# Kernel optimization log

Measured on AMD Instinct MI355X. Metric: run time of the kernel, lower is better.

The kernel has to match this reference:

```python
import jax, jax.numpy as jnp
import numpy as np

N_NODES = 50000
N_EDGES = 1600000
IN_DIM = 128
OUT_DIM = 128


def setup_inputs() -> dict:
    key = jax.random.key(0)
    k_h, k_e, k_wm, k_wu, k_bu = jax.random.split(key, 5)
    h = jax.random.normal(k_h, (N_NODES, IN_DIM), dtype=jnp.float32)
    edge_index = jax.random.randint(k_e, (2, N_EDGES), 0, N_NODES, dtype=jnp.int64)
    # nn.Linear weights: W_msg [out, in] no bias; W_upd [out, in+out] with bias
    s1 = 1.0 / np.sqrt(IN_DIM)
    s2 = 1.0 / np.sqrt(IN_DIM + OUT_DIM)
    W_msg = jax.random.uniform(k_wm, (OUT_DIM, IN_DIM), jnp.float32, -s1, s1)
    W_upd = jax.random.uniform(k_wu, (OUT_DIM, IN_DIM + OUT_DIM), jnp.float32, -s2, s2)
    b_upd = jax.random.uniform(k_bu, (OUT_DIM,), jnp.float32, -s2, s2)
    return {"h": h, "edge_index": edge_index, "W_msg": W_msg, "W_upd": W_upd, "b_upd": b_upd}


def reference(h, edge_index, W_msg, W_upd, b_upd):
    src, dst = edge_index[0], edge_index[1]
    # gather -> linear: messages [E, out_dim]
    messages = jnp.einsum("ei,oi->eo", h[src], W_msg)
    # scatter-add aggregation into [N, out_dim]
    agg = jax.ops.segment_sum(messages, dst, num_segments=h.shape[0])
    # concat -> linear -> relu
    hu = jnp.concatenate([h, agg], axis=1)
    return jax.nn.relu(jnp.einsum("ni,oi->no", hu, W_upd) + b_upd)
```

## Files before the change

### kernel.cpp

```cpp
#include <hip/hip_runtime.h>
#include <hip/hip_bf16.h>

#define NN   50000
#define NE   1600000
#define D    128
#define NBUK 391
#define CAP  5120
#define EPB  4096
#define ASTR 136
#define PREP_BLKS 3125
#define WPREP_BLKS 32

typedef __attribute__((ext_vector_type(8))) short short8;
typedef __attribute__((ext_vector_type(4))) float f32x4;

__device__ __forceinline__ unsigned short f2b(float x) {
  unsigned u = __float_as_uint(x);
  u += 0x7fffu + ((u >> 16) & 1u);
  return (unsigned short)(u >> 16);
}
__device__ __forceinline__ float b2f(unsigned v) {
  return __uint_as_float(v << 16);
}
__device__ __forceinline__ float b2fh(unsigned v) {
  return __uint_as_float(v & 0xffff0000u);
}

__global__ __launch_bounds__(512) void fused_k(const float* __restrict__ h,
                                               unsigned short* __restrict__ hb,
                                               int* __restrict__ gcur,
                                               const float* __restrict__ Wm,
                                               const float* __restrict__ Wu,
                                               unsigned short* __restrict__ W1b,
                                               unsigned short* __restrict__ Wcb,
                                               const int* __restrict__ ei,
                                               unsigned* __restrict__ ebuf) {
  __shared__ int cnt[NBUK];
  __shared__ int off[NBUK];
  __shared__ int nz;
  const int blk = blockIdx.x, tid = threadIdx.x;

  if (blk >= NBUK) {
    if (blk < NBUK + PREP_BLKS) {
      int i = (blk - NBUK) * 512 + tid;
      float4 x = ((const float4*)h)[i];
      ushort4 o;
      o.x = f2b(x.x); o.y = f2b(x.y); o.z = f2b(x.z); o.w = f2b(x.w);
      ((ushort4*)hb)[i] = o;
    } else {
      int t2 = (blk - NBUK - PREP_BLKS) * 512 + tid;
      if (t2 < 16384) {
        int o = t2 >> 7, j = t2 & 127;
        W1b[t2] = f2b(Wu[o * 256 + j]);
        float acc = 0.f;
#pragma unroll 4
        for (int k = 0; k < 128; ++k)
          acc += Wu[o * 256 + 128 + k] * Wm[k * 128 + j];
        Wcb[t2] = f2b(acc);
      }
    }
    return;
  }

  if (tid == 0) nz = 0;
  if (tid < NBUK) cnt[tid] = 0;
  __syncthreads();
  if (tid < 256) {
    int idx = 1 + 2 * (tid * (NE / 256));
    if (ei[idx] != 0) atomicOr(&nz, 1);
  }
  __syncthreads();
  const int f = (nz == 0);

  const int e0 = blk * EPB + tid * 8;
  unsigned pk[8]; int bk[8]; int lr[8];
  if (e0 + 8 <= NE) {
    int sv[8], dv[8];
    if (f) {
      const int4* ps = (const int4*)(ei + 2 * (size_t)e0);
      const int4* pd = (const int4*)(ei + 2 * (size_t)NE + 2 * (size_t)e0);
      int4 a = ps[0], b = ps[1], c = ps[2], d = ps[3];
      sv[0]=a.x; sv[1]=a.z; sv[2]=b.x; sv[3]=b.z; sv[4]=c.x; sv[5]=c.z; sv[6]=d.x; sv[7]=d.z;
      a = pd[0]; b = pd[1]; c = pd[2]; d = pd[3];
      dv[0]=a.x; dv[1]=a.z; dv[2]=b.x; dv[3]=b.z; dv[4]=c.x; dv[5]=c.z; dv[6]=d.x; dv[7]=d.z;
    } else {
      const int4* ps = (const int4*)(ei + e0);
      const int4* pd = (const int4*)(ei + (size_t)NE + e0);
      int4 a = ps[0], b = ps[1];
      sv[0]=a.x; sv[1]=a.y; sv[2]=a.z; sv[3]=a.w; sv[4]=b.x; sv[5]=b.y; sv[6]=b.z; sv[7]=b.w;
      a = pd[0]; b = pd[1];
      dv[0]=a.x; dv[1]=a.y; dv[2]=a.z; dv[3]=a.w; dv[4]=b.x; dv[5]=b.y; dv[6]=b.z; dv[7]=b.w;
    }
#pragma unroll
    for (int j = 0; j < 8; ++j) {
      bk[j] = dv[j] >> 7;
      pk[j] = (unsigned)sv[j] | ((unsigned)(dv[j] & 127) << 16);
      lr[j] = atomicAdd(&cnt[bk[j]], 1);
    }
  } else {
    for (int j = 0; j < 8; ++j) {
      int e = e0 + j;
      bk[j] = -1;
      if (e < NE) {
        int src = f ? ei[2 * (size_t)e] : ei[e];
        int dst = f ? ei[2 * ((size_t)NE + e)] : ei[NE + e];
        bk[j] = dst >> 7;
        pk[j] = (unsigned)src | ((unsigned)(dst & 127) << 16);
        lr[j] = atomicAdd(&cnt[bk[j]], 1);
      }
    }
  }
  __syncthreads();
  if (tid < NBUK)
    off[tid] = cnt[tid] ? atomicAdd(&gcur[tid], cnt[tid]) : 0;
  __syncthreads();
#pragma unroll
  for (int j = 0; j < 8; ++j) {
    if (bk[j] >= 0) {
      int idx = off[bk[j]] + lr[j];
      if (idx < CAP) ebuf[(size_t)bk[j] * CAP + idx] = pk[j];
    }
  }
}

__global__ __launch_bounds__(512, 6) void sortagg_k(const unsigned* __restrict__ ebuf,
                                                    const int* __restrict__ gcur,
                                                    const unsigned short* __restrict__ hb,
                                                    const unsigned short* __restrict__ W1b,
                                                    const unsigned short* __restrict__ Wcb,
                                                    const float* __restrict__ bias,
                                                    float* __restrict__ out) {
  __shared__ unsigned short srt[CAP];
  __shared__ __align__(16) unsigned short aggL[128 * ASTR];
  __shared__ int cnt[128];
  __shared__ int ofs[129];
  __shared__ int cur[128];
  __shared__ int wsum[2];
  const int b = blockIdx.x, tid = threadIdx.x;
  const int lane = tid & 63, wv = tid >> 6;
  if (tid < 128) cnt[tid] = 0;
  __syncthreads();
  const int count = min(gcur[b], CAP);
  const unsigned* eb = ebuf + (size_t)b * CAP;
  for (int e = tid; e < count; e += 512)
    atomicAdd(&cnt[eb[e] >> 16], 1);
  __syncthreads();
  int v = 0, s = 0;
  if (tid < 128) {
    v = cnt[tid]; s = v;
#pragma unroll
    for (int d = 1; d < 64; d <<= 1) {
      int t = __shfl_up(s, d, 64);
      if (lane >= d) s += t;
    }
    if (lane == 63) wsum[wv] = s;
  }
  __syncthreads();
  if (tid < 128) {
    int excl = (wv ? wsum[0] : 0) + s - v;
    ofs[tid] = excl;
    cur[tid] = excl;
  }
  if (tid == 0) ofs[128] = count;
  __syncthreads();
  for (int e = tid; e < count; e += 512) {
    unsigned p = eb[e];
    int slot = atomicAdd(&cur[p >> 16], 1);
    srt[slot] = (unsigned short)(p & 0xffffu);
  }
  __syncthreads();

  const int q = lane >> 4;
  const int r = lane & 15;
  const unsigned short* hbl = hb + r * 8;
#pragma unroll 1
  for (int k = 0; k < 16; ++k) {
    const int n = wv * 16 + k;
    const int beg = ofs[n], end = ofs[n + 1];
    float a0=0.f,a1=0.f,a2=0.f,a3=0.f,a4=0.f,a5=0.f,a6=0.f,a7=0.f;
    int e = beg;
    for (; e + 32 <= end; e += 32) {
      uint4 vv[8];
#pragma unroll
      for (int j = 0; j < 8; ++j)
        vv[j] = *(const uint4*)(hbl + (size_t)srt[e + 4 * j + q] * D);
#pragma unroll
      for (int j = 0; j < 8; ++j) {
        a0 += b2f(vv[j].x & 0xffffu); a1 += b2fh(vv[j].x);
        a2 += b2f(vv[j].y & 0xffffu); a3 += b2fh(vv[j].y);
        a4 += b2f(vv[j].z & 0xffffu); a5 += b2fh(vv[j].z);
        a6 += b2f(vv[j].w & 0xffffu); a7 += b2fh(vv[j].w);
      }
    }
    for (; e < end; e += 4) {
      int edge = e + q;
      int ce = min(edge, end - 1);
      uint4 vv = *(const uint4*)(hbl + (size_t)srt[ce] * D);
      if (edge >= end) { vv.x = 0u; vv.y = 0u; vv.z = 0u; vv.w = 0u; }
      a0 += b2f(vv.x & 0xffffu); a1 += b2fh(vv.x);
      a2 += b2f(vv.y & 0xffffu); a3 += b2fh(vv.y);
      a4 += b2f(vv.z & 0xffffu); a5 += b2fh(vv.z);
      a6 += b2f(vv.w & 0xffffu); a7 += b2fh(vv.w);
    }
    a0 += __shfl_xor(a0, 16, 64); a0 += __shfl_xor(a0, 32, 64);
    a1 += __shfl_xor(a1, 16, 64); a1 += __shfl_xor(a1, 32, 64);
    a2 += __shfl_xor(a2, 16, 64); a2 += __shfl_xor(a2, 32, 64);
    a3 += __shfl_xor(a3, 16, 64); a3 += __shfl_xor(a3, 32, 64);
    a4 += __shfl_xor(a4, 16, 64); a4 += __shfl_xor(a4, 32, 64);
    a5 += __shfl_xor(a5, 16, 64); a5 += __shfl_xor(a5, 32, 64);
    a6 += __shfl_xor(a6, 16, 64); a6 += __shfl_xor(a6, 32, 64);
    a7 += __shfl_xor(a7, 16, 64); a7 += __shfl_xor(a7, 32, 64);
    if (lane < 16) {
      uint4 o;
      o.x = (unsigned)f2b(a0) | ((unsigned)f2b(a1) << 16);
      o.y = (unsigned)f2b(a2) | ((unsigned)f2b(a3) << 16);
      o.z = (unsigned)f2b(a4) | ((unsigned)f2b(a5) << 16);
      o.w = (unsigned)f2b(a6) | ((unsigned)f2b(a7) << 16);
      *(uint4*)(aggL + n * ASTR + r * 8) = o;
    }
  }
  __syncthreads();

  const int rr = lane & 15, g = lane >> 4;
  const int rowL = wv * 16 + rr;
  const int nodeA = min(b * 128 + rowL, NN - 1);

  f32x4 acc[8];
#pragma unroll
  for (int t = 0; t < 8; ++t) acc[t] = (f32x4){0.f, 0.f, 0.f, 0.f};

#pragma unroll
  for (int c = 0; c < 8; ++c) {
    const int k0 = (c & 3) * 32 + g * 8;
    short8 a;
    if (c < 4) {
      a = *(const short8*)(hb + (size_t)nodeA * D + k0);
    } else {
      a = *(const short8*)(aggL + rowL * ASTR + k0);
    }
    const unsigned short* W = (c < 4) ? W1b : Wcb;
#pragma unroll
    for (int t = 0; t < 8; ++t) {
      short8 bfr = *(const short8*)(W + (size_t)(t * 16 + rr) * D + k0);
      acc[t] = __builtin_amdgcn_mfma_f32_16x16x32_bf16(a, bfr, acc[t], 0, 0, 0);
    }
  }

#pragma unroll
  for (int t = 0; t < 8; ++t) {
    const int col = t * 16 + rr;
    const float bv = bias[col];
#pragma unroll
    for (int j = 0; j < 4; ++j) {
      const int orow = b * 128 + wv * 16 + g * 4 + j;
      if (orow < NN) {
        float vv = acc[t][j] + bv;
        out[(size_t)orow * D + col] = vv > 0.f ? vv : 0.f;
      }
    }
  }
}

extern "C" void kernel_launch(void* const* d_in, const int* in_sizes, int n_in,
                              void* d_out, int out_size, void* d_ws, size_t ws_size,
                              hipStream_t stream) {
  const float* h  = (const float*)d_in[0];
  const int*   ei = (const int*)d_in[1];
  const float* Wm = (const float*)d_in[2];
  const float* Wu = (const float*)d_in[3];
  const float* bu = (const float*)d_in[4];
  float* out = (float*)d_out;

  char* ws = (char*)d_ws;
  unsigned short* hb   = (unsigned short*)(ws);
  unsigned*       ebuf = (unsigned*)(ws + 12800000);
  int*            gcur = (int*)(ws + 20807680);
  unsigned short* W1b  = (unsigned short*)(ws + 20809728);
  unsigned short* Wcb  = (unsigned short*)(ws + 20842496);

  hipMemsetAsync(gcur, 0, NBUK * sizeof(int), stream);
  fused_k<<<NBUK + PREP_BLKS + WPREP_BLKS, 512, 0, stream>>>(
      h, hb, gcur, Wm, Wu, W1b, Wcb, ei, ebuf);
  sortagg_k<<<NBUK, 512, 0, stream>>>(ebuf, gcur, hb, W1b, Wcb, bu, out);
}
```

Baseline: 126.4 us.

## Halve destination bucket size to 64 nodes, doubling aggregation blocks

Destination buckets shrink from 128 to 64 nodes, so the sort/aggregate kernel launches 782 blocks instead of 391. Each wave now aggregates 8 nodes with a 16-edge gather unroll, and the MFMA epilogue splits output columns across wave pairs. The aim is to fill more of the GPU's compute units and shorten each block's serial aggregation work. The cost is more global bucket atomics, smaller per-block tiles, and a tighter per-bucket capacity that could overflow on skewed degree distributions.

New measurement: 121.3 us. -4.0%, faster.

```diff
diff --git a/kernel.cpp b/kernel.cpp
--- a/kernel.cpp
+++ b/kernel.cpp
@@ -4,9 +4,10 @@
 #define NN   50000
 #define NE   1600000
 #define D    128
-#define NBUK 391
-#define CAP  5120
+#define NBK  782
+#define CAP2 2816
 #define EPB  4096
+#define FILLB 391
 #define ASTR 136
 #define PREP_BLKS 3125
 #define WPREP_BLKS 32
@@ -35,20 +36,20 @@
                                                unsigned short* __restrict__ Wcb,
                                                const int* __restrict__ ei,
                                                unsigned* __restrict__ ebuf) {
-  __shared__ int cnt[NBUK];
-  __shared__ int off[NBUK];
+  __shared__ int cnt[NBK];
+  __shared__ int off[NBK];
   __shared__ int nz;
   const int blk = blockIdx.x, tid = threadIdx.x;
 
-  if (blk >= NBUK) {
-    if (blk < NBUK + PREP_BLKS) {
-      int i = (blk - NBUK) * 512 + tid;
+  if (blk >= FILLB) {
+    if (blk < FILLB + PREP_BLKS) {
+      int i = (blk - FILLB) * 512 + tid;
       float4 x = ((const float4*)h)[i];
       ushort4 o;
       o.x = f2b(x.x); o.y = f2b(x.y); o.z = f2b(x.z); o.w = f2b(x.w);
       ((ushort4*)hb)[i] = o;
     } else {
-      int t2 = (blk - NBUK - PREP_BLKS) * 512 + tid;
+      int t2 = (blk - FILLB - PREP_BLKS) * 512 + tid;
       if (t2 < 16384) {
         int o = t2 >> 7, j = t2 & 127;
         W1b[t2] = f2b(Wu[o * 256 + j]);
@@ -63,7 +64,7 @@
   }
 
   if (tid == 0) nz = 0;
-  if (tid < NBUK) cnt[tid] = 0;
+  for (int t = tid; t < NBK; t += 512) cnt[t] = 0;
   __syncthreads();
   if (tid < 256) {
     int idx = 1 + 2 * (tid * (NE / 256));
@@ -93,8 +94,8 @@
     }
 #pragma unroll
     for (int j = 0; j < 8; ++j) {
-      bk[j] = dv[j] >> 7;
-      pk[j] = (unsigned)sv[j] | ((unsigned)(dv[j] & 127) << 16);
+      bk[j] = dv[j] >> 6;
+      pk[j] = (unsigned)sv[j] | ((unsigned)(dv[j] & 63) << 16);
       lr[j] = atomicAdd(&cnt[bk[j]], 1);
     }
   } else {
@@ -104,64 +105,57 @@
       if (e < NE) {
         int src = f ? ei[2 * (size_t)e] : ei[e];
         int dst = f ? ei[2 * ((size_t)NE + e)] : ei[NE + e];
-        bk[j] = dst >> 7;
-        pk[j] = (unsigned)src | ((unsigned)(dst & 127) << 16);
+        bk[j] = dst >> 6;
+        pk[j] = (unsigned)src | ((unsigned)(dst & 63) << 16);
         lr[j] = atomicAdd(&cnt[bk[j]], 1);
       }
     }
   }
   __syncthreads();
-  if (tid < NBUK)
-    off[tid] = cnt[tid] ? atomicAdd(&gcur[tid], cnt[tid]) : 0;
+  for (int t = tid; t < NBK; t += 512)
+    off[t] = cnt[t] ? atomicAdd(&gcur[t], cnt[t]) : 0;
   __syncthreads();
 #pragma unroll
   for (int j = 0; j < 8; ++j) {
     if (bk[j] >= 0) {
       int idx = off[bk[j]] + lr[j];
-      if (idx < CAP) ebuf[(size_t)bk[j] * CAP + idx] = pk[j];
-    }
-  }
-}
-
-__global__ __launch_bounds__(512, 6) void sortagg_k(const unsigned* __restrict__ ebuf,
+      if (idx < CAP2) ebuf[(size_t)bk[j] * CAP2 + idx] = pk[j];
+    }
+  }
+}
+
+__global__ __launch_bounds__(512, 4) void sortagg_k(const unsigned* __restrict__ ebuf,
                                                     const int* __restrict__ gcur,
                                                     const unsigned short* __restrict__ hb,
                                                     const unsigned short* __restrict__ W1b,
                                                     const unsigned short* __restrict__ Wcb,
                                                     const float* __restrict__ bias,
                                                     float* __restrict__ out) {
-  __shared__ unsigned short srt[CAP];
-  __shared__ __align__(16) unsigned short aggL[128 * ASTR];
-  __shared__ int cnt[128];
-  __shared__ int ofs[129];
-  __shared__ int cur[128];
-  __shared__ int wsum[2];
+  __shared__ unsigned short srt[CAP2];
+  __shared__ __align__(16) unsigned short aggL[64 * ASTR];
+  __shared__ int cnt[64];
+  __shared__ int ofs[65];
+  __shared__ int cur[64];
   const int b = blockIdx.x, tid = threadIdx.x;
   const int lane = tid & 63, wv = tid >> 6;
-  if (tid < 128) cnt[tid] = 0;
-  __syncthreads();
-  const int count = min(gcur[b], CAP);
-  const unsigned* eb = ebuf + (size_t)b * CAP;
+  if (tid < 64) cnt[tid] = 0;
+  __syncthreads();
+  const int count = min(gcur[b], CAP2);
+  const unsigned* eb = ebuf + (size_t)b * CAP2;
   for (int e = tid; e < count; e += 512)
     atomicAdd(&cnt[eb[e] >> 16], 1);
   __syncthreads();
-  int v = 0, s = 0;
-  if (tid < 128) {
-    v = cnt[tid]; s = v;
+  if (wv == 0) {
+    int v = cnt[lane], s = v;
 #pragma unroll
     for (int d = 1; d < 64; d <<= 1) {
       int t = __shfl_up(s, d, 64);
       if (lane >= d) s += t;
     }
-    if (lane == 63) wsum[wv] = s;
-  }
-  __syncthreads();
-  if (tid < 128) {
-    int excl = (wv ? wsum[0] : 0) + s - v;
-    ofs[tid] = excl;
-    cur[tid] = excl;
-  }
-  if (tid == 0) ofs[128] = count;
+    ofs[lane] = s - v;
+    cur[lane] = s - v;
+    if (lane == 63) ofs[64] = count;
+  }
   __syncthreads();
   for (int e = tid; e < count; e += 512) {
     unsigned p = eb[e];
@@ -174,18 +168,18 @@
   const int r = lane & 15;
   const unsigned short* hbl = hb + r * 8;
 #pragma unroll 1
-  for (int k = 0; k < 16; ++k) {
-    const int n = wv * 16 + k;
+  for (int k = 0; k < 8; ++k) {
+    const int n = wv * 8 + k;
     const int beg = ofs[n], end = ofs[n + 1];
     float a0=0.f,a1=0.f,a2=0.f,a3=0.f,a4=0.f,a5=0.f,a6=0.f,a7=0.f;
     int e = beg;
-    for (; e + 32 <= end; e += 32) {
-      uint4 vv[8];
-#pragma unroll
-      for (int j = 0; j < 8; ++j)
+    for (; e + 16 <= end; e += 16) {
+      uint4 vv[4];
+#pragma unroll
+      for (int j = 0; j < 4; ++j)
         vv[j] = *(const uint4*)(hbl + (size_t)srt[e + 4 * j + q] * D);
 #pragma unroll
-      for (int j = 0; j < 8; ++j) {
+      for (int j = 0; j < 4; ++j) {
         a0 += b2f(vv[j].x & 0xffffu); a1 += b2fh(vv[j].x);
         a2 += b2f(vv[j].y & 0xffffu); a3 += b2fh(vv[j].y);
         a4 += b2f(vv[j].z & 0xffffu); a5 += b2fh(vv[j].z);
@@ -222,12 +216,14 @@
   __syncthreads();
 
   const int rr = lane & 15, g = lane >> 4;
-  const int rowL = wv * 16 + rr;
-  const int nodeA = min(b * 128 + rowL, NN - 1);
-
-  f32x4 acc[8];
-#pragma unroll
-  for (int t = 0; t < 8; ++t) acc[t] = (f32x4){0.f, 0.f, 0.f, 0.f};
+  const int rtile = wv >> 1;
+  const int t0 = (wv & 1) * 4;
+  const int rowL = rtile * 16 + rr;
+  const int nodeA = min(b * 64 + rowL, NN - 1);
+
+  f32x4 acc[4];
+#pragma unroll
+  for (int t = 0; t < 4; ++t) acc[t] = (f32x4){0.f, 0.f, 0.f, 0.f};
 
 #pragma unroll
   for (int c = 0; c < 8; ++c) {
@@ -240,21 +236,21 @@
     }
     const unsigned short* W = (c < 4) ? W1b : Wcb;
 #pragma unroll
-    for (int t = 0; t < 8; ++t) {
-      short8 bfr = *(const short8*)(W + (size_t)(t * 16 + rr) * D + k0);
-      acc[t] = __builtin_amdgcn_mfma_f32_16x16x32_bf16(a, bfr, acc[t], 0, 0, 0);
-    }
-  }
-
-#pragma unroll
-  for (int t = 0; t < 8; ++t) {
-    const int col = t * 16 + rr;
+    for (int tt = 0; tt < 4; ++tt) {
+      short8 bfr = *(const short8*)(W + (size_t)((t0 + tt) * 16 + rr) * D + k0);
+      acc[tt] = __builtin_amdgcn_mfma_f32_16x16x32_bf16(a, bfr, acc[tt], 0, 0, 0);
+    }
+  }
+
+#pragma unroll
+  for (int tt = 0; tt < 4; ++tt) {
+    const int col = (t0 + tt) * 16 + rr;
     const float bv = bias[col];
 #pragma unroll
     for (int j = 0; j < 4; ++j) {
-      const int orow = b * 128 + wv * 16 + g * 4 + j;
+      const int orow = b * 64 + rtile * 16 + g * 4 + j;
       if (orow < NN) {
-        float vv = acc[t][j] + bv;
+        float vv = acc[tt][j] + bv;
         out[(size_t)orow * D + col] = vv > 0.f ? vv : 0.f;
       }
     }
@@ -274,12 +270,12 @@
   char* ws = (char*)d_ws;
   unsigned short* hb   = (unsigned short*)(ws);
   unsigned*       ebuf = (unsigned*)(ws + 12800000);
-  int*            gcur = (int*)(ws + 20807680);
-  unsigned short* W1b  = (unsigned short*)(ws + 20809728);
-  unsigned short* Wcb  = (unsigned short*)(ws + 20842496);
-
-  hipMemsetAsync(gcur, 0, NBUK * sizeof(int), stream);
-  fused_k<<<NBUK + PREP_BLKS + WPREP_BLKS, 512, 0, stream>>>(
+  int*            gcur = (int*)(ws + 21608448);
+  unsigned short* W1b  = (unsigned short*)(ws + 21611576 + 8);
+  unsigned short* Wcb  = (unsigned short*)(ws + 21644352);
+
+  hipMemsetAsync(gcur, 0, NBK * sizeof(int), stream);
+  fused_k<<<FILLB + PREP_BLKS + WPREP_BLKS, 512, 0, stream>>>(
       h, hb, gcur, Wm, Wu, W1b, Wcb, ei, ebuf);
-  sortagg_k<<<NBUK, 512, 0, stream>>>(ebuf, gcur, hb, W1b, Wcb, bu, out);
-}
+  sortagg_k<<<NBK, 512, 0, stream>>>(ebuf, gcur, hb, W1b, Wcb, bu, out);
+}
```
